# Performance work log

Hardware: AMD Instinct MI355X
Metric: run time of the kernel (lower is better)

Reference implementation:

```python
import jax, jax.numpy as jnp
import numpy as np

NUM_HEADS = 16


def setup_inputs() -> dict:
    key = jax.random.key(0)
    ks = jax.random.split(key, 7)
    B_, N, C = 512, 64, 512
    x = jax.random.normal(ks[0], (B_, N, C), dtype=jnp.float32)
    attn_bias = jax.random.normal(ks[1], (NUM_HEADS, N, N), dtype=jnp.float32)
    mask = jax.random.normal(ks[2], (B_, N, N), dtype=jnp.float32)
    qkv_w = jax.random.normal(ks[3], (3 * C, C), dtype=jnp.float32) * (C ** -0.5)
    qkv_b = jax.random.normal(ks[4], (3 * C,), dtype=jnp.float32) * 0.02
    proj_w = jax.random.normal(ks[5], (C, C), dtype=jnp.float32) * (C ** -0.5)
    proj_b = jax.random.normal(ks[6], (C,), dtype=jnp.float32) * 0.02
    return {"x": x, "attn_bias": attn_bias, "mask": mask,
            "qkv_w": qkv_w, "qkv_b": qkv_b, "proj_w": proj_w, "proj_b": proj_b}


def reference(x, attn_bias, mask, qkv_w, qkv_b, proj_w, proj_b):
    B_, N, C = x.shape
    H = NUM_HEADS
    hd = C // H
    scale = hd ** -0.5
    # qkv projection: (B_, N, 3, H, hd) -> (3, B_, H, N, hd)
    qkv = (x @ qkv_w.T + qkv_b).reshape(B_, N, 3, H, hd)
    qkv = jnp.transpose(qkv, (2, 0, 3, 1, 4))
    q, k, v = qkv[0], qkv[1], qkv[2]
    attn = jnp.einsum('bhnd,bhmd->bhnm', q * scale, k)  # (B_, H, N, N)
    attn = attn + attn_bias            # (H, N, N) broadcasts over batch
    attn = attn + mask[:, None]        # (B_, 1, N, N)
    attn = jax.nn.softmax(attn, axis=-1)
    out = jnp.einsum('bhnm,bhmd->bhnd', attn, v)
    out = jnp.transpose(out, (0, 2, 1, 3)).reshape(B_, N, C)
    return out @ proj_w.T + proj_b
```

## Files before the change

kernel.cpp:

```cpp
#include <hip/hip_runtime.h>
#include <stdint.h>

typedef __attribute__((ext_vector_type(8))) __bf16 bf16x8;
typedef __attribute__((ext_vector_type(4))) float f32x4;
typedef __attribute__((ext_vector_type(4))) float fl4;
typedef __attribute__((ext_vector_type(8))) unsigned short us8;
typedef __attribute__((ext_vector_type(4))) unsigned short us4;

__device__ __forceinline__ unsigned short f2bf(float f) {
  union { float f; unsigned int u; } v;
  v.f = f;
  unsigned int r = v.u + 0x7FFFu + ((v.u >> 16) & 1u);
  return (unsigned short)(r >> 16);
}

#define GLOAD_LDS16(g, l)                                                   \
  __builtin_amdgcn_global_load_lds(                                         \
      (const __attribute__((address_space(1))) void*)(g),                   \
      (__attribute__((address_space(3))) void*)(l), 16, 0, 0)

__global__ void f32_to_bf16_kernel(const float* __restrict__ in,
                                   unsigned short* __restrict__ out, int n) {
  int i = (blockIdx.x * blockDim.x + threadIdx.x) * 4;
  if (i + 3 < n) {
    fl4 v = *(const fl4*)(in + i);
    us4 o;
    o[0] = f2bf(v[0]);
    o[1] = f2bf(v[1]);
    o[2] = f2bf(v[2]);
    o[3] = f2bf(v[3]);
    *(us4*)(out + i) = o;
  }
}

template <bool OUT_BF16>
__global__ __launch_bounds__(256, 2) void gemm128_kernel(
    const unsigned short* __restrict__ A, const unsigned short* __restrict__ B,
    const float* __restrict__ bias, void* __restrict__ Cout, int M, int N,
    int K, int NT) {
  __shared__ __align__(16) unsigned short lds[32768];
  char* base = (char*)lds;

  const int tid = threadIdx.x;
  const int lane = tid & 63;
  const int wid = tid >> 6;
  const int lr = lane & 15;
  const int lg = lane >> 4;
  const int wr = (wid >> 1) * 64;
  const int wc = (wid & 1) * 64;

  const int bid = blockIdx.x;
  const int bm = ((bid & 31) + (bid / (32 * NT)) * 32) << 7;
  const int bn = (((bid >> 5) % NT)) << 7;

  const int srow = tid >> 3;
  const int scolsw = ((tid & 7) << 4) ^ ((srow & 7) << 4);
  const char* Ag = (const char*)A;
  const char* Bg = (const char*)B;
  const size_t Kb = (size_t)K * 2;

#define STAGE(kt, p)                                                          \
  {                                                                           \
    char* la_ = base + (p) * 32768;                                           \
    char* lb_ = la_ + 16384;                                                  \
    _Pragma("unroll") for (int i_ = 0; i_ < 4; ++i_) {                        \
      GLOAD_LDS16(Ag + (size_t)(bm + srow + i_ * 32) * Kb + (kt) * 128 + scolsw, \
                  la_ + srow * 128 + i_ * 4096 + (tid & 7) * 16);             \
      GLOAD_LDS16(Bg + (size_t)(bn + srow + i_ * 32) * Kb + (kt) * 128 + scolsw, \
                  lb_ + srow * 128 + i_ * 4096 + (tid & 7) * 16);             \
    }                                                                         \
  }

  const int swz = (lr & 7) << 4;
  const int ck0 = (lg << 4) ^ swz;
  const int ck1 = (64 + (lg << 4)) ^ swz;

  f32x4 acc[4][4];
#pragma unroll
  for (int m = 0; m < 4; ++m)
#pragma unroll
    for (int n = 0; n < 4; ++n) acc[m][n] = (f32x4){0.f, 0.f, 0.f, 0.f};

  const int nkt = K >> 6;

  STAGE(0, 0);
  __syncthreads();

  for (int kt = 0; kt < nkt; ++kt) {
    const int p = kt & 1;
    if (kt + 1 < nkt) STAGE(kt + 1, p ^ 1);

    const char* la = base + p * 32768;
    const char* lb = la + 16384;
    bf16x8 af[4][2], bfr[4][2];
#pragma unroll
    for (int m = 0; m < 4; ++m) {
      const int arow = (wr + m * 16 + lr) << 7;
      af[m][0] = *(const bf16x8*)(la + arow + ck0);
      af[m][1] = *(const bf16x8*)(la + arow + ck1);
    }
#pragma unroll
    for (int n = 0; n < 4; ++n) {
      const int brow = (wc + n * 16 + lr) << 7;
      bfr[n][0] = *(const bf16x8*)(lb + brow + ck0);
      bfr[n][1] = *(const bf16x8*)(lb + brow + ck1);
    }
#pragma unroll
    for (int kk = 0; kk < 2; ++kk)
#pragma unroll
      for (int m = 0; m < 4; ++m)
#pragma unroll
        for (int n = 0; n < 4; ++n)
          acc[m][n] = __builtin_amdgcn_mfma_f32_16x16x32_bf16(
              af[m][kk], bfr[n][kk], acc[m][n], 0, 0, 0);
    __syncthreads();
  }
#undef STAGE

  const int crow0 = bm + wr + lg * 4;
  const int ccol0 = bn + wc + lr;
#pragma unroll
  for (int n = 0; n < 4; ++n) {
    const int col = ccol0 + n * 16;
    const float bv = bias[col];
#pragma unroll
    for (int m = 0; m < 4; ++m) {
#pragma unroll
      for (int j = 0; j < 4; ++j) {
        const int row = crow0 + m * 16 + j;
        const float val = acc[m][n][j] + bv;
        if (OUT_BF16)
          ((unsigned short*)Cout)[(size_t)row * N + col] = f2bf(val);
        else
          ((float*)Cout)[(size_t)row * N + col] = val;
      }
    }
  }
}

__global__ __launch_bounds__(256, 4) void attn_kernel(
    const unsigned short* __restrict__ qkv, const float* __restrict__ abias,
    const float* __restrict__ mask, unsigned short* __restrict__ out) {
  __shared__ __align__(16) unsigned short lq[64 * 40];
  __shared__ __align__(16) unsigned short lk[64 * 40];
  __shared__ __align__(16) unsigned short lvT[32 * 72];
  __shared__ __align__(16) unsigned short lp[64 * 72];

  const int bid = blockIdx.x;
  const int id2 = (bid & 7) * 1024 + (bid >> 3);
  const int b = id2 >> 4;
  const int h = id2 & 15;
  const int tid = threadIdx.x;
  const int lane = tid & 63;
  const int wid = tid >> 6;
  const int lr = lane & 15;
  const int lg = lane >> 4;
  const int lk8 = lg * 8;

  {
    const int r = tid >> 2;
    const int d0 = (tid & 3) * 8;
    const size_t bse = (size_t)(b * 64 + r) * 1536 + h * 32 + d0;
    us8 qv = *(const us8*)(qkv + bse);
    us8 kv = *(const us8*)(qkv + bse + 512);
    us8 vv = *(const us8*)(qkv + bse + 1024);
    *(us8*)(lq + r * 40 + d0) = qv;
    *(us8*)(lk + r * 40 + d0) = kv;
#pragma unroll
    for (int i = 0; i < 8; ++i) lvT[(d0 + i) * 72 + r] = vv[i];
  }
  __syncthreads();

  f32x4 s[4];
  {
    bf16x8 aq = *(const bf16x8*)(lq + (wid * 16 + lr) * 40 + lk8);
#pragma unroll
    for (int n = 0; n < 4; ++n) {
      bf16x8 bk = *(const bf16x8*)(lk + (n * 16 + lr) * 40 + lk8);
      f32x4 z = {0.f, 0.f, 0.f, 0.f};
      s[n] = __builtin_amdgcn_mfma_f32_16x16x32_bf16(aq, bk, z, 0, 0, 0);
    }
  }
  const float scale = 0.17677669529663687f;
  const int row0 = wid * 16 + lg * 4;
#pragma unroll
  for (int j = 0; j < 4; ++j) {
    const int row = row0 + j;
    const float* ab = abias + (h * 64 + row) * 64 + lr;
    const float* mk = mask + ((size_t)b * 64 + row) * 64 + lr;
#pragma unroll
    for (int n = 0; n < 4; ++n)
      s[n][j] = s[n][j] * scale + ab[n * 16] + mk[n * 16];
  }

  float mx[4], sm[4];
#pragma unroll
  for (int j = 0; j < 4; ++j)
    mx[j] = fmaxf(fmaxf(s[0][j], s[1][j]), fmaxf(s[2][j], s[3][j]));
#pragma unroll
  for (int xm = 1; xm <= 8; xm <<= 1)
#pragma unroll
    for (int j = 0; j < 4; ++j) mx[j] = fmaxf(mx[j], __shfl_xor(mx[j], xm));
#pragma unroll
  for (int j = 0; j < 4; ++j) sm[j] = 0.f;
#pragma unroll
  for (int n = 0; n < 4; ++n)
#pragma unroll
    for (int j = 0; j < 4; ++j) {
      const float e = __expf(s[n][j] - mx[j]);
      s[n][j] = e;
      sm[j] += e;
    }
#pragma unroll
  for (int xm = 1; xm <= 8; xm <<= 1)
#pragma unroll
    for (int j = 0; j < 4; ++j) sm[j] += __shfl_xor(sm[j], xm);
#pragma unroll
  for (int j = 0; j < 4; ++j) sm[j] = 1.f / sm[j];
#pragma unroll
  for (int n = 0; n < 4; ++n)
#pragma unroll
    for (int j = 0; j < 4; ++j)
      lp[(row0 + j) * 72 + n * 16 + lr] = f2bf(s[n][j] * sm[j]);
  __syncthreads();

  f32x4 o[2];
  o[0] = (f32x4){0.f, 0.f, 0.f, 0.f};
  o[1] = o[0];
#pragma unroll
  for (int kk = 0; kk < 2; ++kk) {
    bf16x8 pa = *(const bf16x8*)(lp + (wid * 16 + lr) * 72 + kk * 32 + lk8);
#pragma unroll
    for (int d = 0; d < 2; ++d) {
      bf16x8 vb = *(const bf16x8*)(lvT + (d * 16 + lr) * 72 + kk * 32 + lk8);
      o[d] = __builtin_amdgcn_mfma_f32_16x16x32_bf16(pa, vb, o[d], 0, 0, 0);
    }
  }
#pragma unroll
  for (int d = 0; d < 2; ++d) {
    const int col = h * 32 + d * 16 + lr;
#pragma unroll
    for (int j = 0; j < 4; ++j) {
      const int row = row0 + j;
      out[(size_t)(b * 64 + row) * 512 + col] = f2bf(o[d][j]);
    }
  }
}

extern "C" void kernel_launch(void* const* d_in, const int* in_sizes, int n_in,
                              void* d_out, int out_size, void* d_ws,
                              size_t ws_size, hipStream_t stream) {
  (void)in_sizes; (void)n_in; (void)out_size; (void)ws_size;
  const float* x = (const float*)d_in[0];
  const float* abias = (const float*)d_in[1];
  const float* mask = (const float*)d_in[2];
  const float* qkv_w = (const float*)d_in[3];
  const float* qkv_b = (const float*)d_in[4];
  const float* proj_w = (const float*)d_in[5];
  const float* proj_b = (const float*)d_in[6];

  char* ws = (char*)d_ws;
  unsigned short* ws_x = (unsigned short*)(ws);
  unsigned short* ws_qkv = (unsigned short*)(ws + 33554432);
  unsigned short* ws_wq = (unsigned short*)(ws + 134217728);
  unsigned short* ws_wp = (unsigned short*)(ws + 135790592);
  unsigned short* ws_att = ws_x;

  f32_to_bf16_kernel<<<16384, 256, 0, stream>>>(x, ws_x, 16777216);
  f32_to_bf16_kernel<<<768, 256, 0, stream>>>(qkv_w, ws_wq, 786432);
  f32_to_bf16_kernel<<<256, 256, 0, stream>>>(proj_w, ws_wp, 262144);

  gemm128_kernel<true><<<3072, 256, 0, stream>>>(ws_x, ws_wq, qkv_b, ws_qkv,
                                                 32768, 1536, 512, 12);

  attn_kernel<<<8192, 256, 0, stream>>>(ws_qkv, abias, mask, ws_att);

  gemm128_kernel<false><<<1024, 256, 0, stream>>>(ws_att, ws_wp, proj_b, d_out,
                                                  32768, 512, 512, 4);
}
```

Before: 266.6 us.

## Fuse x conversion into QKV GEMM and fuse attention with output projection

The QKV GEMM now reads fp32 x directly, converting to bf16 in registers before writing to LDS, which drops the separate x conversion pass and its bf16 round trip through global memory. The attention kernel becomes one block per batch element that loops over all 16 heads, two at a time, and keeps the 64x512 attention output in LDS. It then runs the output projection inside the same block, streaming proj_w tiles through registers into LDS. This removes the attention output write and read in global memory but cuts the attention grid to 512 blocks of 512 threads with heavy LDS use, lowering occupancy. The A operand in the GEMM also moves from async global-to-LDS loads to register staging.

```diff
diff --git a/kernel.cpp b/kernel.cpp
--- a/kernel.cpp
+++ b/kernel.cpp
@@ -2,6 +2,7 @@
 #include <stdint.h>
 
 typedef __attribute__((ext_vector_type(8))) __bf16 bf16x8;
+typedef __attribute__((ext_vector_type(4))) __bf16 bf16x4;
 typedef __attribute__((ext_vector_type(4))) float f32x4;
 typedef __attribute__((ext_vector_type(4))) float fl4;
 typedef __attribute__((ext_vector_type(8))) unsigned short us8;
@@ -33,11 +34,10 @@
   }
 }
 
-template <bool OUT_BF16>
-__global__ __launch_bounds__(256, 2) void gemm128_kernel(
-    const unsigned short* __restrict__ A, const unsigned short* __restrict__ B,
-    const float* __restrict__ bias, void* __restrict__ Cout, int M, int N,
-    int K, int NT) {
+__global__ __launch_bounds__(256, 2) void gemm128f_kernel(
+    const float* __restrict__ Af, const unsigned short* __restrict__ B,
+    const float* __restrict__ bias, unsigned short* __restrict__ Cout, int M,
+    int N, int K, int NT) {
   __shared__ __align__(16) unsigned short lds[32768];
   char* base = (char*)lds;
 
@@ -55,20 +55,38 @@
 
   const int srow = tid >> 3;
   const int scolsw = ((tid & 7) << 4) ^ ((srow & 7) << 4);
-  const char* Ag = (const char*)A;
+  const int awch = ((tid & 7) << 4) ^ ((srow & 7) << 4);
   const char* Bg = (const char*)B;
   const size_t Kb = (size_t)K * 2;
 
-#define STAGE(kt, p)                                                          \
-  {                                                                           \
-    char* la_ = base + (p) * 32768;                                           \
-    char* lb_ = la_ + 16384;                                                  \
-    _Pragma("unroll") for (int i_ = 0; i_ < 4; ++i_) {                        \
-      GLOAD_LDS16(Ag + (size_t)(bm + srow + i_ * 32) * Kb + (kt) * 128 + scolsw, \
-                  la_ + srow * 128 + i_ * 4096 + (tid & 7) * 16);             \
-      GLOAD_LDS16(Bg + (size_t)(bn + srow + i_ * 32) * Kb + (kt) * 128 + scolsw, \
-                  lb_ + srow * 128 + i_ * 4096 + (tid & 7) * 16);             \
-    }                                                                         \
+  fl4 fa[4][2];
+
+#define STAGE_B(kt, p)                                                         \
+  {                                                                            \
+    char* lb_ = base + (p)*32768 + 16384;                                      \
+    _Pragma("unroll") for (int i_ = 0; i_ < 4; ++i_) {                         \
+      GLOAD_LDS16(Bg + (size_t)(bn + srow + i_ * 32) * Kb + (kt)*128 + scolsw, \
+                  lb_ + srow * 128 + i_ * 4096 + (tid & 7) * 16);              \
+    }                                                                          \
+  }
+#define LOAD_A(kt)                                                             \
+  _Pragma("unroll") for (int i_ = 0; i_ < 4; ++i_) {                           \
+    const float* ap_ =                                                         \
+        Af + (size_t)(bm + srow + i_ * 32) * K + (kt)*64 + (tid & 7) * 8;      \
+    fa[i_][0] = *(const fl4*)(ap_);                                            \
+    fa[i_][1] = *(const fl4*)(ap_ + 4);                                        \
+  }
+#define WRITE_A(p)                                                             \
+  {                                                                            \
+    char* la_ = base + (p)*32768;                                              \
+    _Pragma("unroll") for (int i_ = 0; i_ < 4; ++i_) {                         \
+      bf16x8 w_;                                                               \
+      _Pragma("unroll") for (int e_ = 0; e_ < 4; ++e_) {                       \
+        w_[e_] = (__bf16)fa[i_][0][e_];                                        \
+        w_[e_ + 4] = (__bf16)fa[i_][1][e_];                                    \
+      }                                                                        \
+      *(bf16x8*)(la_ + (srow + i_ * 32) * 128 + awch) = w_;                    \
+    }                                                                          \
   }
 
   const int swz = (lr & 7) << 4;
@@ -83,13 +101,17 @@
 
   const int nkt = K >> 6;
 
-  STAGE(0, 0);
+  STAGE_B(0, 0);
+  LOAD_A(0);
+  WRITE_A(0);
   __syncthreads();
 
   for (int kt = 0; kt < nkt; ++kt) {
     const int p = kt & 1;
-    if (kt + 1 < nkt) STAGE(kt + 1, p ^ 1);
-
+    if (kt + 1 < nkt) {
+      STAGE_B(kt + 1, p ^ 1);
+      LOAD_A(kt + 1);
+    }
     const char* la = base + p * 32768;
     const char* lb = la + 16384;
     bf16x8 af[4][2], bfr[4][2];
@@ -113,9 +135,12 @@
         for (int n = 0; n < 4; ++n)
           acc[m][n] = __builtin_amdgcn_mfma_f32_16x16x32_bf16(
               af[m][kk], bfr[n][kk], acc[m][n], 0, 0, 0);
-    __syncthreads();
-  }
-#undef STAGE
+    if (kt + 1 < nkt) WRITE_A(p ^ 1);
+    __syncthreads();
+  }
+#undef STAGE_B
+#undef LOAD_A
+#undef WRITE_A
 
   const int crow0 = bm + wr + lg * 4;
   const int ccol0 = bn + wc + lr;
@@ -128,121 +153,199 @@
 #pragma unroll
       for (int j = 0; j < 4; ++j) {
         const int row = crow0 + m * 16 + j;
-        const float val = acc[m][n][j] + bv;
-        if (OUT_BF16)
-          ((unsigned short*)Cout)[(size_t)row * N + col] = f2bf(val);
-        else
-          ((float*)Cout)[(size_t)row * N + col] = val;
-      }
-    }
-  }
-}
-
-__global__ __launch_bounds__(256, 4) void attn_kernel(
+        Cout[(size_t)row * N + col] = f2bf(acc[m][n][j] + bv);
+      }
+    }
+  }
+}
+
+__global__ __launch_bounds__(512, 1) void attnproj_kernel(
     const unsigned short* __restrict__ qkv, const float* __restrict__ abias,
-    const float* __restrict__ mask, unsigned short* __restrict__ out) {
-  __shared__ __align__(16) unsigned short lq[64 * 40];
-  __shared__ __align__(16) unsigned short lk[64 * 40];
-  __shared__ __align__(16) unsigned short lvT[32 * 72];
-  __shared__ __align__(16) unsigned short lp[64 * 72];
-
-  const int bid = blockIdx.x;
-  const int id2 = (bid & 7) * 1024 + (bid >> 3);
-  const int b = id2 >> 4;
-  const int h = id2 & 15;
+    const float* __restrict__ mask, const unsigned short* __restrict__ wp,
+    const float* __restrict__ pbias, float* __restrict__ out) {
+  __shared__ __align__(16) unsigned short SH[33280 + 24576];
+  unsigned short* AO = SH;
+
   const int tid = threadIdx.x;
+  const int g = tid >> 8;
+  const int gtid = tid & 255;
+  const int gwid = (tid >> 6) & 3;
   const int lane = tid & 63;
-  const int wid = tid >> 6;
   const int lr = lane & 15;
   const int lg = lane >> 4;
   const int lk8 = lg * 8;
-
-  {
-    const int r = tid >> 2;
-    const int d0 = (tid & 3) * 8;
-    const size_t bse = (size_t)(b * 64 + r) * 1536 + h * 32 + d0;
-    us8 qv = *(const us8*)(qkv + bse);
-    us8 kv = *(const us8*)(qkv + bse + 512);
-    us8 vv = *(const us8*)(qkv + bse + 1024);
-    *(us8*)(lq + r * 40 + d0) = qv;
-    *(us8*)(lk + r * 40 + d0) = kv;
-#pragma unroll
-    for (int i = 0; i < 8; ++i) lvT[(d0 + i) * 72 + r] = vv[i];
-  }
-  __syncthreads();
-
-  f32x4 s[4];
-  {
-    bf16x8 aq = *(const bf16x8*)(lq + (wid * 16 + lr) * 40 + lk8);
-#pragma unroll
-    for (int n = 0; n < 4; ++n) {
-      bf16x8 bk = *(const bf16x8*)(lk + (n * 16 + lr) * 40 + lk8);
-      f32x4 z = {0.f, 0.f, 0.f, 0.f};
-      s[n] = __builtin_amdgcn_mfma_f32_16x16x32_bf16(aq, bk, z, 0, 0, 0);
-    }
-  }
+  const int b = blockIdx.x;
+
+  unsigned short* gb = SH + 33280 + g * 12032;
+  unsigned short* lq = gb;
+  unsigned short* lk = gb + 2560;
+  unsigned short* lvT = gb + 5120;
+  unsigned short* lp = gb + 7424;
+
   const float scale = 0.17677669529663687f;
-  const int row0 = wid * 16 + lg * 4;
-#pragma unroll
-  for (int j = 0; j < 4; ++j) {
-    const int row = row0 + j;
-    const float* ab = abias + (h * 64 + row) * 64 + lr;
-    const float* mk = mask + ((size_t)b * 64 + row) * 64 + lr;
-#pragma unroll
-    for (int n = 0; n < 4; ++n)
-      s[n][j] = s[n][j] * scale + ab[n * 16] + mk[n * 16];
-  }
-
-  float mx[4], sm[4];
-#pragma unroll
-  for (int j = 0; j < 4; ++j)
-    mx[j] = fmaxf(fmaxf(s[0][j], s[1][j]), fmaxf(s[2][j], s[3][j]));
-#pragma unroll
-  for (int xm = 1; xm <= 8; xm <<= 1)
-#pragma unroll
-    for (int j = 0; j < 4; ++j) mx[j] = fmaxf(mx[j], __shfl_xor(mx[j], xm));
-#pragma unroll
-  for (int j = 0; j < 4; ++j) sm[j] = 0.f;
-#pragma unroll
-  for (int n = 0; n < 4; ++n)
-#pragma unroll
-    for (int j = 0; j < 4; ++j) {
-      const float e = __expf(s[n][j] - mx[j]);
-      s[n][j] = e;
-      sm[j] += e;
-    }
-#pragma unroll
-  for (int xm = 1; xm <= 8; xm <<= 1)
-#pragma unroll
-    for (int j = 0; j < 4; ++j) sm[j] += __shfl_xor(sm[j], xm);
-#pragma unroll
-  for (int j = 0; j < 4; ++j) sm[j] = 1.f / sm[j];
-#pragma unroll
-  for (int n = 0; n < 4; ++n)
-#pragma unroll
-    for (int j = 0; j < 4; ++j)
-      lp[(row0 + j) * 72 + n * 16 + lr] = f2bf(s[n][j] * sm[j]);
-  __syncthreads();
-
-  f32x4 o[2];
-  o[0] = (f32x4){0.f, 0.f, 0.f, 0.f};
-  o[1] = o[0];
-#pragma unroll
-  for (int kk = 0; kk < 2; ++kk) {
-    bf16x8 pa = *(const bf16x8*)(lp + (wid * 16 + lr) * 72 + kk * 32 + lk8);
-#pragma unroll
-    for (int d = 0; d < 2; ++d) {
-      bf16x8 vb = *(const bf16x8*)(lvT + (d * 16 + lr) * 72 + kk * 32 + lk8);
-      o[d] = __builtin_amdgcn_mfma_f32_16x16x32_bf16(pa, vb, o[d], 0, 0, 0);
-    }
-  }
-#pragma unroll
-  for (int d = 0; d < 2; ++d) {
-    const int col = h * 32 + d * 16 + lr;
+  const int row0 = gwid * 16 + lg * 4;
+
+  for (int hr = 0; hr < 8; ++hr) {
+    const int h = hr * 2 + g;
+    {
+      const int r = gtid >> 2;
+      const int d0 = (gtid & 3) * 8;
+      const size_t bse = (size_t)(b * 64 + r) * 1536 + h * 32 + d0;
+      us8 qv = *(const us8*)(qkv + bse);
+      us8 kv = *(const us8*)(qkv + bse + 512);
+      us8 vv = *(const us8*)(qkv + bse + 1024);
+      *(us8*)(lq + r * 40 + d0) = qv;
+      *(us8*)(lk + r * 40 + d0) = kv;
+#pragma unroll
+      for (int i = 0; i < 8; ++i) lvT[(d0 + i) * 72 + r] = vv[i];
+    }
+    __syncthreads();
+
+    f32x4 s[4];
+    {
+      bf16x8 aq = *(const bf16x8*)(lq + (gwid * 16 + lr) * 40 + lk8);
+#pragma unroll
+      for (int n = 0; n < 4; ++n) {
+        bf16x8 bk = *(const bf16x8*)(lk + (n * 16 + lr) * 40 + lk8);
+        f32x4 z = {0.f, 0.f, 0.f, 0.f};
+        s[n] = __builtin_amdgcn_mfma_f32_16x16x32_bf16(aq, bk, z, 0, 0, 0);
+      }
+    }
 #pragma unroll
     for (int j = 0; j < 4; ++j) {
       const int row = row0 + j;
-      out[(size_t)(b * 64 + row) * 512 + col] = f2bf(o[d][j]);
+      const float* ab = abias + (h * 64 + row) * 64 + lr;
+      const float* mk = mask + ((size_t)b * 64 + row) * 64 + lr;
+#pragma unroll
+      for (int n = 0; n < 4; ++n)
+        s[n][j] = s[n][j] * scale + ab[n * 16] + mk[n * 16];
+    }
+
+    float mx[4], sm[4];
+#pragma unroll
+    for (int j = 0; j < 4; ++j)
+      mx[j] = fmaxf(fmaxf(s[0][j], s[1][j]), fmaxf(s[2][j], s[3][j]));
+#pragma unroll
+    for (int xm = 1; xm <= 8; xm <<= 1)
+#pragma unroll
+      for (int j = 0; j < 4; ++j) mx[j] = fmaxf(mx[j], __shfl_xor(mx[j], xm));
+#pragma unroll
+    for (int j = 0; j < 4; ++j) sm[j] = 0.f;
+#pragma unroll
+    for (int n = 0; n < 4; ++n)
+#pragma unroll
+      for (int j = 0; j < 4; ++j) {
+        const float e = __expf(s[n][j] - mx[j]);
+        s[n][j] = e;
+        sm[j] += e;
+      }
+#pragma unroll
+    for (int xm = 1; xm <= 8; xm <<= 1)
+#pragma unroll
+      for (int j = 0; j < 4; ++j) sm[j] += __shfl_xor(sm[j], xm);
+#pragma unroll
+    for (int j = 0; j < 4; ++j) sm[j] = 1.f / sm[j];
+#pragma unroll
+    for (int n = 0; n < 4; ++n)
+#pragma unroll
+      for (int j = 0; j < 4; ++j)
+        lp[(row0 + j) * 72 + n * 16 + lr] = f2bf(s[n][j] * sm[j]);
+    __syncthreads();
+
+    f32x4 o[2];
+    o[0] = (f32x4){0.f, 0.f, 0.f, 0.f};
+    o[1] = o[0];
+#pragma unroll
+    for (int kk = 0; kk < 2; ++kk) {
+      bf16x8 pa = *(const bf16x8*)(lp + (gwid * 16 + lr) * 72 + kk * 32 + lk8);
+#pragma unroll
+      for (int d = 0; d < 2; ++d) {
+        bf16x8 vb = *(const bf16x8*)(lvT + (d * 16 + lr) * 72 + kk * 32 + lk8);
+        o[d] = __builtin_amdgcn_mfma_f32_16x16x32_bf16(pa, vb, o[d], 0, 0, 0);
+      }
+    }
+#pragma unroll
+    for (int d = 0; d < 2; ++d) {
+      const int col = h * 32 + d * 16 + lr;
+#pragma unroll
+      for (int j = 0; j < 4; ++j) AO[(row0 + j) * 520 + col] = f2bf(o[d][j]);
+    }
+    __syncthreads();
+  }
+
+  unsigned short* lwp = SH + 33280;
+  const int wv = tid >> 6;
+  const int prow = tid >> 2;
+  const int pc = (tid & 3) * 8;
+
+  f32x4 pacc[4][4];
+#pragma unroll
+  for (int m = 0; m < 4; ++m)
+#pragma unroll
+    for (int n = 0; n < 4; ++n) pacc[m][n] = (f32x4){0.f, 0.f, 0.f, 0.f};
+
+  us8 wreg[4];
+#pragma unroll
+  for (int s0 = 0; s0 < 4; ++s0)
+    wreg[s0] = *(const us8*)(wp + (size_t)(prow + s0 * 128) * 512 + pc);
+#pragma unroll
+  for (int s0 = 0; s0 < 4; ++s0) {
+    const int ro = (prow + s0 * 128) * 44 + pc;
+    *(us4*)(lwp + ro) = (us4){wreg[s0][0], wreg[s0][1], wreg[s0][2], wreg[s0][3]};
+    *(us4*)(lwp + ro + 4) = (us4){wreg[s0][4], wreg[s0][5], wreg[s0][6], wreg[s0][7]};
+  }
+  __syncthreads();
+
+  for (int kt = 0; kt < 16; ++kt) {
+    if (kt < 15) {
+#pragma unroll
+      for (int s0 = 0; s0 < 4; ++s0)
+        wreg[s0] = *(const us8*)(wp + (size_t)(prow + s0 * 128) * 512 +
+                                 (kt + 1) * 32 + pc);
+    }
+    bf16x8 af[4], bfr[4];
+#pragma unroll
+    for (int mq = 0; mq < 4; ++mq)
+      af[mq] = *(const bf16x8*)(AO + (mq * 16 + lr) * 520 + kt * 32 + lk8);
+#pragma unroll
+    for (int n = 0; n < 4; ++n) {
+      const int ro = (wv * 64 + n * 16 + lr) * 44 + lk8;
+      union { bf16x8 v8; bf16x4 v4[2]; } u;
+      u.v4[0] = *(const bf16x4*)(lwp + ro);
+      u.v4[1] = *(const bf16x4*)(lwp + ro + 4);
+      bfr[n] = u.v8;
+    }
+#pragma unroll
+    for (int mq = 0; mq < 4; ++mq)
+#pragma unroll
+      for (int n = 0; n < 4; ++n)
+        pacc[mq][n] = __builtin_amdgcn_mfma_f32_16x16x32_bf16(
+            af[mq], bfr[n], pacc[mq][n], 0, 0, 0);
+    __syncthreads();
+    if (kt < 15) {
+#pragma unroll
+      for (int s0 = 0; s0 < 4; ++s0) {
+        const int ro = (prow + s0 * 128) * 44 + pc;
+        *(us4*)(lwp + ro) =
+            (us4){wreg[s0][0], wreg[s0][1], wreg[s0][2], wreg[s0][3]};
+        *(us4*)(lwp + ro + 4) =
+            (us4){wreg[s0][4], wreg[s0][5], wreg[s0][6], wreg[s0][7]};
+      }
+      __syncthreads();
+    }
+  }
+
+#pragma unroll
+  for (int n = 0; n < 4; ++n) {
+    const int col = wv * 64 + n * 16 + lr;
+    const float bv = pbias[col];
+#pragma unroll
+    for (int mq = 0; mq < 4; ++mq) {
+#pragma unroll
+      for (int j = 0; j < 4; ++j) {
+        const int row = mq * 16 + lg * 4 + j;
+        out[(size_t)(b * 64 + row) * 512 + col] = pacc[mq][n][j] + bv;
+      }
     }
   }
 }
@@ -260,21 +363,16 @@
   const float* proj_b = (const float*)d_in[6];
 
   char* ws = (char*)d_ws;
-  unsigned short* ws_x = (unsigned short*)(ws);
-  unsigned short* ws_qkv = (unsigned short*)(ws + 33554432);
-  unsigned short* ws_wq = (unsigned short*)(ws + 134217728);
-  unsigned short* ws_wp = (unsigned short*)(ws + 135790592);
-  unsigned short* ws_att = ws_x;
-
-  f32_to_bf16_kernel<<<16384, 256, 0, stream>>>(x, ws_x, 16777216);
+  unsigned short* ws_qkv = (unsigned short*)(ws);
+  unsigned short* ws_wq = (unsigned short*)(ws + 100663296);
+  unsigned short* ws_wp = (unsigned short*)(ws + 102236160);
+
   f32_to_bf16_kernel<<<768, 256, 0, stream>>>(qkv_w, ws_wq, 786432);
   f32_to_bf16_kernel<<<256, 256, 0, stream>>>(proj_w, ws_wp, 262144);
 
-  gemm128_kernel<true><<<3072, 256, 0, stream>>>(ws_x, ws_wq, qkv_b, ws_qkv,
-                                                 32768, 1536, 512, 12);
-
-  attn_kernel<<<8192, 256, 0, stream>>>(ws_qkv, abias, mask, ws_att);
-
-  gemm128_kernel<false><<<1024, 256, 0, stream>>>(ws_att, ws_wp, proj_b, d_out,
-                                                  32768, 512, 512, 4);
-}
+  gemm128f_kernel<<<3072, 256, 0, stream>>>(x, ws_wq, qkv_b, ws_qkv, 32768,
+                                            1536, 512, 12);
+
+  attnproj_kernel<<<512, 512, 0, stream>>>(ws_qkv, abias, mask, ws_wp, proj_b,
+                                           (float*)d_out);
+}
```

Result: slower. 301.7 us (+13.2%).

## Use 8-wave GEMM blocks and merge the three bf16 conversion launches

Applied to the files above, without the earlier changes.

The 128x128 GEMM tile now runs with 512 threads (8 waves, each computing 64x32), which halves accumulators per wave and doubles the waves resident per tile to hide LDS and MFMA latency. Each thread now stages two 16-byte global-to-LDS loads per operand instead of four. The three separate fp32-to-bf16 conversion launches are merged into one kernel that picks its source buffer by index range, removing two launches. The cost is more waves contending at the barrier and a smaller per-wave tile, which lowers register-level reuse of the A fragments.

```diff
diff --git a/kernel.cpp b/kernel.cpp
--- a/kernel.cpp
+++ b/kernel.cpp
@@ -19,22 +19,34 @@
       (const __attribute__((address_space(1))) void*)(g),                   \
       (__attribute__((address_space(3))) void*)(l), 16, 0, 0)
 
-__global__ void f32_to_bf16_kernel(const float* __restrict__ in,
-                                   unsigned short* __restrict__ out, int n) {
-  int i = (blockIdx.x * blockDim.x + threadIdx.x) * 4;
-  if (i + 3 < n) {
-    fl4 v = *(const fl4*)(in + i);
-    us4 o;
-    o[0] = f2bf(v[0]);
-    o[1] = f2bf(v[1]);
-    o[2] = f2bf(v[2]);
-    o[3] = f2bf(v[3]);
-    *(us4*)(out + i) = o;
-  }
+__global__ void convert_all_kernel(const float* __restrict__ x,
+                                   const float* __restrict__ wq,
+                                   const float* __restrict__ wp,
+                                   unsigned short* __restrict__ ox,
+                                   unsigned short* __restrict__ owq,
+                                   unsigned short* __restrict__ owp) {
+  const int i = (blockIdx.x * blockDim.x + threadIdx.x) * 4;
+  const float* src;
+  unsigned short* dst;
+  int off;
+  if (i < 16777216) {
+    src = x; dst = ox; off = i;
+  } else if (i < 17563648) {
+    src = wq; dst = owq; off = i - 16777216;
+  } else {
+    src = wp; dst = owp; off = i - 17563648;
+  }
+  fl4 v = *(const fl4*)(src + off);
+  us4 o;
+  o[0] = f2bf(v[0]);
+  o[1] = f2bf(v[1]);
+  o[2] = f2bf(v[2]);
+  o[3] = f2bf(v[3]);
+  *(us4*)(dst + off) = o;
 }
 
 template <bool OUT_BF16>
-__global__ __launch_bounds__(256, 2) void gemm128_kernel(
+__global__ __launch_bounds__(512, 4) void gemm128_kernel(
     const unsigned short* __restrict__ A, const unsigned short* __restrict__ B,
     const float* __restrict__ bias, void* __restrict__ Cout, int M, int N,
     int K, int NT) {
@@ -46,40 +58,40 @@
   const int wid = tid >> 6;
   const int lr = lane & 15;
   const int lg = lane >> 4;
-  const int wr = (wid >> 1) * 64;
-  const int wc = (wid & 1) * 64;
+  const int wm = wid >> 2;
+  const int wn = wid & 3;
 
   const int bid = blockIdx.x;
   const int bm = ((bid & 31) + (bid / (32 * NT)) * 32) << 7;
   const int bn = (((bid >> 5) % NT)) << 7;
 
   const int srow = tid >> 3;
-  const int scolsw = ((tid & 7) << 4) ^ ((srow & 7) << 4);
+  const int scsw = ((tid & 7) << 4) ^ ((srow & 7) << 4);
   const char* Ag = (const char*)A;
   const char* Bg = (const char*)B;
   const size_t Kb = (size_t)K * 2;
 
-#define STAGE(kt, p)                                                          \
-  {                                                                           \
-    char* la_ = base + (p) * 32768;                                           \
-    char* lb_ = la_ + 16384;                                                  \
-    _Pragma("unroll") for (int i_ = 0; i_ < 4; ++i_) {                        \
-      GLOAD_LDS16(Ag + (size_t)(bm + srow + i_ * 32) * Kb + (kt) * 128 + scolsw, \
-                  la_ + srow * 128 + i_ * 4096 + (tid & 7) * 16);             \
-      GLOAD_LDS16(Bg + (size_t)(bn + srow + i_ * 32) * Kb + (kt) * 128 + scolsw, \
-                  lb_ + srow * 128 + i_ * 4096 + (tid & 7) * 16);             \
-    }                                                                         \
+#define STAGE(kt, p)                                                           \
+  {                                                                            \
+    char* la_ = base + (p)*32768;                                              \
+    char* lb_ = la_ + 16384;                                                   \
+    _Pragma("unroll") for (int i_ = 0; i_ < 2; ++i_) {                         \
+      GLOAD_LDS16(Ag + (size_t)(bm + srow + i_ * 64) * Kb + (kt)*128 + scsw,   \
+                  la_ + (srow + i_ * 64) * 128 + (tid & 7) * 16);              \
+      GLOAD_LDS16(Bg + (size_t)(bn + srow + i_ * 64) * Kb + (kt)*128 + scsw,   \
+                  lb_ + (srow + i_ * 64) * 128 + (tid & 7) * 16);              \
+    }                                                                          \
   }
 
   const int swz = (lr & 7) << 4;
   const int ck0 = (lg << 4) ^ swz;
   const int ck1 = (64 + (lg << 4)) ^ swz;
 
-  f32x4 acc[4][4];
+  f32x4 acc[4][2];
 #pragma unroll
   for (int m = 0; m < 4; ++m)
 #pragma unroll
-    for (int n = 0; n < 4; ++n) acc[m][n] = (f32x4){0.f, 0.f, 0.f, 0.f};
+    for (int n = 0; n < 2; ++n) acc[m][n] = (f32x4){0.f, 0.f, 0.f, 0.f};
 
   const int nkt = K >> 6;
 
@@ -92,16 +104,16 @@
 
     const char* la = base + p * 32768;
     const char* lb = la + 16384;
-    bf16x8 af[4][2], bfr[4][2];
+    bf16x8 af[4][2], bfr[2][2];
 #pragma unroll
     for (int m = 0; m < 4; ++m) {
-      const int arow = (wr + m * 16 + lr) << 7;
+      const int arow = (wm * 64 + m * 16 + lr) << 7;
       af[m][0] = *(const bf16x8*)(la + arow + ck0);
       af[m][1] = *(const bf16x8*)(la + arow + ck1);
     }
 #pragma unroll
-    for (int n = 0; n < 4; ++n) {
-      const int brow = (wc + n * 16 + lr) << 7;
+    for (int n = 0; n < 2; ++n) {
+      const int brow = (wn * 32 + n * 16 + lr) << 7;
       bfr[n][0] = *(const bf16x8*)(lb + brow + ck0);
       bfr[n][1] = *(const bf16x8*)(lb + brow + ck1);
     }
@@ -110,17 +122,17 @@
 #pragma unroll
       for (int m = 0; m < 4; ++m)
 #pragma unroll
-        for (int n = 0; n < 4; ++n)
+        for (int n = 0; n < 2; ++n)
           acc[m][n] = __builtin_amdgcn_mfma_f32_16x16x32_bf16(
               af[m][kk], bfr[n][kk], acc[m][n], 0, 0, 0);
     __syncthreads();
   }
 #undef STAGE
 
-  const int crow0 = bm + wr + lg * 4;
-  const int ccol0 = bn + wc + lr;
-#pragma unroll
-  for (int n = 0; n < 4; ++n) {
+  const int crow0 = bm + wm * 64 + lg * 4;
+  const int ccol0 = bn + wn * 32 + lr;
+#pragma unroll
+  for (int n = 0; n < 2; ++n) {
     const int col = ccol0 + n * 16;
     const float bv = bias[col];
 #pragma unroll
@@ -266,15 +278,14 @@
   unsigned short* ws_wp = (unsigned short*)(ws + 135790592);
   unsigned short* ws_att = ws_x;
 
-  f32_to_bf16_kernel<<<16384, 256, 0, stream>>>(x, ws_x, 16777216);
-  f32_to_bf16_kernel<<<768, 256, 0, stream>>>(qkv_w, ws_wq, 786432);
-  f32_to_bf16_kernel<<<256, 256, 0, stream>>>(proj_w, ws_wp, 262144);
-
-  gemm128_kernel<true><<<3072, 256, 0, stream>>>(ws_x, ws_wq, qkv_b, ws_qkv,
+  convert_all_kernel<<<17408, 256, 0, stream>>>(x, qkv_w, proj_w, ws_x, ws_wq,
+                                                ws_wp);
+
+  gemm128_kernel<true><<<3072, 512, 0, stream>>>(ws_x, ws_wq, qkv_b, ws_qkv,
                                                  32768, 1536, 512, 12);
 
   attn_kernel<<<8192, 256, 0, stream>>>(ws_qkv, abias, mask, ws_att);
 
-  gemm128_kernel<false><<<1024, 256, 0, stream>>>(ws_att, ws_wp, proj_b, d_out,
+  gemm128_kernel<false><<<1024, 512, 0, stream>>>(ws_att, ws_wp, proj_b, d_out,
                                                   32768, 512, 512, 4);
 }
```

After: 259.9 us. -2.5%, faster.
